# Kernel tuning notes

Measured on AMD Instinct MI355X. Metric: run time of the kernel, lower is better.

The kernel has to match this reference:

```python
import jax, jax.numpy as jnp
import numpy as np

B, T, I, H = 1024, 64, 64, 1024
FUTURE = 16


def lstm_cell(x_t, h, c, Wih, Whh, b_ih, b_hh):
    # torch LSTMCell gate order: i, f, g, o; weights are (4H, in)
    gates = x_t @ Wih.T + h @ Whh.T + b_ih + b_hh  # (B, 4H)
    i, f, g, o = jnp.split(gates, 4, axis=-1)
    i = jax.nn.sigmoid(i)
    f = jax.nn.sigmoid(f)
    g = jnp.tanh(g)
    o = jax.nn.sigmoid(o)
    c_new = f * c + i * g
    h_new = o * jnp.tanh(c_new)
    return h_new, c_new


def setup_inputs() -> dict:
    key = jax.random.key(0)
    ks = jax.random.split(key, 12)
    s1 = 1.0 / np.sqrt(H)
    inp = {
        "x": jax.random.normal(ks[0], (B, T, I), dtype=jnp.float32),
        "W_ih1": jax.random.uniform(ks[1], (4 * H, I), jnp.float32, -s1, s1),
        "W_hh1": jax.random.uniform(ks[2], (4 * H, H), jnp.float32, -s1, s1),
        "b_ih1": jax.random.uniform(ks[3], (4 * H,), jnp.float32, -s1, s1),
        "b_hh1": jax.random.uniform(ks[4], (4 * H,), jnp.float32, -s1, s1),
        "W_ih2": jax.random.uniform(ks[5], (4 * H, H), jnp.float32, -s1, s1),
        "W_hh2": jax.random.uniform(ks[6], (4 * H, H), jnp.float32, -s1, s1),
        "b_ih2": jax.random.uniform(ks[7], (4 * H,), jnp.float32, -s1, s1),
        "b_hh2": jax.random.uniform(ks[8], (4 * H,), jnp.float32, -s1, s1),
        "W_lin": jax.random.uniform(ks[9], (I, H), jnp.float32, -s1, s1),
        "b_lin": jax.random.uniform(ks[10], (I,), jnp.float32, -s1, s1),
        "future": FUTURE,
    }
    return inp


def reference(x, W_ih1, W_hh1, b_ih1, b_hh1, W_ih2, W_hh2, b_ih2, b_hh2,
              W_lin, b_lin, future):
    b_size = x.shape[0]
    zeros = jnp.zeros((b_size, H), dtype=x.dtype)

    def two_layer_step(h1, c1, h2, c2, x_t):
        h1, c1 = lstm_cell(x_t, h1, c1, W_ih1, W_hh1, b_ih1, b_hh1)
        h2, c2 = lstm_cell(h1, h2, c2, W_ih2, W_hh2, b_ih2, b_hh2)
        out = h2 @ W_lin.T + b_lin  # (B, I)
        return h1, c1, h2, c2, out

    def step(carry, x_t):
        h1, c1, h2, c2 = carry
        h1, c1, h2, c2, out = two_layer_step(h1, c1, h2, c2, x_t)
        return (h1, c1, h2, c2), out

    xs = jnp.transpose(x, (1, 0, 2))  # (T, B, I)
    carry, outs = jax.lax.scan(step, (zeros, zeros, zeros, zeros), xs)

    if future > 0:
        def fstep(carry, _):
            h1, c1, h2, c2, out = carry
            h1, c1, h2, c2, out = two_layer_step(h1, c1, h2, c2, out)
            return (h1, c1, h2, c2, out), out

        h1, c1, h2, c2 = carry
        _, fouts = jax.lax.scan(fstep, (h1, c1, h2, c2, outs[-1]),
                                None, length=future)
        outs = jnp.concatenate([outs, fouts], axis=0)

    return jnp.transpose(outs, (1, 0, 2))  # (B, T+future, I)
```

## Files before the change

### kernel.cpp

```cpp
#include <hip/hip_runtime.h>


#define B_   1024
#define T_   64
#define I_   64
#define H_   1024
#define FUT_ 16
#define NST_ (T_ + FUT_)
#define SROW 2176

typedef _Float16 half8_t  __attribute__((ext_vector_type(8)));
typedef float    float4_t __attribute__((ext_vector_type(4)));

__device__ __forceinline__ float sigmoid_f(float x) {
    x = fminf(fmaxf(x, -30.f), 30.f);
    return __fdividef(1.f, 1.f + __expf(-x));
}
__device__ __forceinline__ float tanh_f(float x) {
    x = fminf(fmaxf(x, -15.f), 15.f);
    float e = __expf(2.f * x);
    return 1.f - 2.f * __fdividef(1.f, e + 1.f);
}

__global__ void convert_all(const float* __restrict__ x,
    const float* __restrict__ Wih1, const float* __restrict__ Whh1,
    const float* __restrict__ bih1, const float* __restrict__ bhh1,
    const float* __restrict__ Wih2, const float* __restrict__ Whh2,
    const float* __restrict__ bih2, const float* __restrict__ bhh2,
    const float* __restrict__ Wlin,
    _Float16* __restrict__ W1p, _Float16* __restrict__ W2p,
    _Float16* __restrict__ Wlp,
    _Float16* __restrict__ S0x, _Float16* __restrict__ S1x,
    float* __restrict__ b1, float* __restrict__ b2)
{
    size_t idx = (size_t)blockIdx.x * 256 + threadIdx.x;
    const size_t nc1 = 589824;
    const size_t nc2 = 1048576;
    const size_t nc3 = 8192;
    const size_t nx  = 65536;
    if (idx < nc1) {
        int c = (int)idx;
        int lane = c & 63, g = (c >> 6) & 3, rem = c >> 8;
        int j = rem % 36, hgrp = rem / 36;
        int row = (g << 10) + hgrp * 16 + (lane & 15);
        int kb = j * 32 + (lane >> 4) * 8;
        _Float16* o = &W1p[(size_t)c * 8];
        if (kb < 1024) {
            #pragma unroll
            for (int i = 0; i < 8; ++i) o[i] = (_Float16)Whh1[(size_t)row * 1024 + kb + i];
        } else if (kb < 1088) {
            #pragma unroll
            for (int i = 0; i < 8; ++i) o[i] = (_Float16)Wih1[row * 64 + (kb - 1024) + i];
        } else {
            #pragma unroll
            for (int i = 0; i < 8; ++i) o[i] = (_Float16)0.f;
        }
    } else if ((idx -= nc1) < nc2) {
        int c = (int)idx;
        int lane = c & 63, g = (c >> 6) & 3, rem = c >> 8;
        int j = rem & 63, hgrp = rem >> 6;
        int row = (g << 10) + hgrp * 16 + (lane & 15);
        int kb = j * 32 + (lane >> 4) * 8;
        _Float16* o = &W2p[(size_t)c * 8];
        if (kb < 1024) {
            #pragma unroll
            for (int i = 0; i < 8; ++i) o[i] = (_Float16)Wih2[(size_t)row * 1024 + kb + i];
        } else {
            #pragma unroll
            for (int i = 0; i < 8; ++i) o[i] = (_Float16)Whh2[(size_t)row * 1024 + kb - 1024 + i];
        }
    } else if ((idx -= nc2) < nc3) {
        int c = (int)idx;
        int lane = c & 63, j = (c >> 6) & 31, hgrp = c >> 11;
        int row = hgrp * 16 + (lane & 15);
        int kb = j * 32 + (lane >> 4) * 8;
        _Float16* o = &Wlp[(size_t)c * 8];
        #pragma unroll
        for (int i = 0; i < 8; ++i) o[i] = (_Float16)Wlin[(size_t)row * 1024 + kb + i];
    } else if ((idx -= nc3) < nx) {
        int b = (int)(idx >> 6), i = (int)(idx & 63);
        S0x[(size_t)b * SROW + i] = (_Float16)x[(size_t)b * (T_ * I_) + i];
    } else if ((idx -= nx) < nx) {
        int b = (int)(idx >> 6), i = (int)(idx & 63);
        S1x[(size_t)b * SROW + i] = (_Float16)x[(size_t)b * (T_ * I_) + 64 + i];
    } else if ((idx -= nx) < 4096) {
        b1[idx] = bih1[idx] + bhh1[idx];
    } else if ((idx -= 4096) < 4096) {
        b2[idx] = bih2[idx] + bhh2[idx];
    }
}

__device__ __forceinline__ void gemm_body(_Float16 (*sA)[136],
    const _Float16* __restrict__ Alo, const _Float16* __restrict__ Ahi,
    const _Float16* __restrict__ Wp, const int iters, const int Ksh,
    const float* __restrict__ bias, float* __restrict__ cvec,
    _Float16* __restrict__ hdst, const int unit)
{
    const int tid = threadIdx.x;
    const int lane = tid & 63, w = tid >> 6;
    const int hw = w & 1, kh = w >> 1;
    const int lr = lane & 15, lq = lane >> 4;
    const int ht = unit & 31, mt = unit >> 5;
    const int h0 = ht * 32, m0 = mt * 64;
    const int hgrp = ht * 2 + hw;

    const char* wptr = (const char*)Wp
        + ((size_t)hgrp * (2 * Ksh) + (size_t)kh * Ksh) * 4096
        + (size_t)lane * 16;

    const int srow0 = tid >> 4, grp = tid & 15;
    const _Float16* abase = (grp < 8 ? Alo : Ahi) + (size_t)(grp & 7) * 8;
    const _Float16* arow = abase + (size_t)(m0 + srow0) * SROW;

    float4_t acc[4][4];
    #pragma unroll
    for (int g = 0; g < 4; ++g)
        #pragma unroll
        for (int rt = 0; rt < 4; ++rt)
            #pragma unroll
            for (int e = 0; e < 4; ++e) acc[g][rt][e] = 0.f;

    for (int i = 0; i < iters; ++i) {
        #pragma unroll
        for (int s = 0; s < 4; ++s)
            *(half8_t*)&sA[srow0 + s * 16][grp * 8] =
                *(const half8_t*)(arow + (size_t)s * 16 * SROW + i * 64);
        __syncthreads();
        #pragma unroll
        for (int ks = 0; ks < 2; ++ks) {
            half8_t af[4], bf[4];
            #pragma unroll
            for (int g = 0; g < 4; ++g)
                bf[g] = *(const half8_t*)(wptr + (ks * 4 + g) * 1024);
            #pragma unroll
            for (int rt = 0; rt < 4; ++rt)
                af[rt] = *(const half8_t*)&sA[rt * 16 + lr][kh * 64 + ks * 32 + lq * 8];
            #pragma unroll
            for (int g = 0; g < 4; ++g)
                #pragma unroll
                for (int rt = 0; rt < 4; ++rt)
                    acc[g][rt] = __builtin_amdgcn_mfma_f32_16x16x32_f16(
                        af[rt], bf[g], acc[g][rt], 0, 0, 0);
        }
        wptr += 8192;
        __syncthreads();
    }

    float* scr = (float*)&sA[0][0];
    #pragma unroll
    for (int gp = 0; gp < 2; ++gp) {
        if (kh == 1) {
            #pragma unroll
            for (int g2 = 0; g2 < 2; ++g2)
                #pragma unroll
                for (int rt = 0; rt < 4; ++rt) {
                    int slot = ((hw * 2 + g2) * 4 + rt) * 64 + lane;
                    *(float4_t*)&scr[slot * 4] = acc[gp * 2 + g2][rt];
                }
        }
        __syncthreads();
        if (kh == 0) {
            #pragma unroll
            for (int g2 = 0; g2 < 2; ++g2)
                #pragma unroll
                for (int rt = 0; rt < 4; ++rt) {
                    int slot = ((hw * 2 + g2) * 4 + rt) * 64 + lane;
                    acc[gp * 2 + g2][rt] += *(const float4_t*)&scr[slot * 4];
                }
        }
        __syncthreads();
    }
    if (kh != 0) return;

    const int j = h0 + hw * 16 + lr;
    const float bi = bias[j], bff = bias[1024 + j];
    const float bg = bias[2048 + j], bo = bias[3072 + j];
    #pragma unroll
    for (int rt = 0; rt < 4; ++rt) {
        #pragma unroll
        for (int e = 0; e < 4; ++e) {
            const int brow = m0 + rt * 16 + lq * 4 + e;
            float gi = sigmoid_f(acc[0][rt][e] + bi);
            float gf = sigmoid_f(acc[1][rt][e] + bff);
            float gg = tanh_f(acc[2][rt][e] + bg);
            float go = sigmoid_f(acc[3][rt][e] + bo);
            const size_t ci = (size_t)brow * 1024 + j;
            float cn = gf * cvec[ci] + gi * gg;
            cvec[ci] = cn;
            hdst[(size_t)brow * SROW + j] = (_Float16)(go * tanh_f(cn));
        }
    }
}

__device__ __forceinline__ void proj_body(_Float16 (*sA)[136],
    const _Float16* __restrict__ A, const _Float16* __restrict__ Wp,
    const float* __restrict__ blin, float* __restrict__ outp,
    _Float16* __restrict__ xdst, const int unit)
{
    const int iters = 8, Ksh = 16;
    const int tid = threadIdx.x;
    const int lane = tid & 63, w = tid >> 6;
    const int hw = w & 1, kh = w >> 1;
    const int lr = lane & 15, lq = lane >> 4;
    const int ht = unit & 1, mt = unit >> 1;
    const int h0 = ht * 32, m0 = mt * 64;
    const int hgrp = ht * 2 + hw;

    const char* wptr = (const char*)Wp
        + ((size_t)hgrp * (2 * Ksh) + (size_t)kh * Ksh) * 1024
        + (size_t)lane * 16;

    const int srow0 = tid >> 4, grp = tid & 15;
    const _Float16* abase = A + (grp >> 3) * 512 + (size_t)(grp & 7) * 8;
    const _Float16* arow = abase + (size_t)(m0 + srow0) * SROW;

    float4_t acc[4];
    #pragma unroll
    for (int rt = 0; rt < 4; ++rt)
        #pragma unroll
        for (int e = 0; e < 4; ++e) acc[rt][e] = 0.f;

    for (int i = 0; i < iters; ++i) {
        #pragma unroll
        for (int s = 0; s < 4; ++s)
            *(half8_t*)&sA[srow0 + s * 16][grp * 8] =
                *(const half8_t*)(arow + (size_t)s * 16 * SROW + i * 64);
        __syncthreads();
        #pragma unroll
        for (int ks = 0; ks < 2; ++ks) {
            half8_t af[4], bf;
            bf = *(const half8_t*)(wptr + ks * 1024);
            #pragma unroll
            for (int rt = 0; rt < 4; ++rt)
                af[rt] = *(const half8_t*)&sA[rt * 16 + lr][kh * 64 + ks * 32 + lq * 8];
            #pragma unroll
            for (int rt = 0; rt < 4; ++rt)
                acc[rt] = __builtin_amdgcn_mfma_f32_16x16x32_f16(
                    af[rt], bf, acc[rt], 0, 0, 0);
        }
        wptr += 2048;
        __syncthreads();
    }

    float* scr = (float*)&sA[0][0];
    if (kh == 1) {
        #pragma unroll
        for (int rt = 0; rt < 4; ++rt) {
            int slot = (hw * 4 + rt) * 64 + lane;
            *(float4_t*)&scr[slot * 4] = acc[rt];
        }
    }
    __syncthreads();
    if (kh != 0) return;
    #pragma unroll
    for (int rt = 0; rt < 4; ++rt) {
        int slot = (hw * 4 + rt) * 64 + lane;
        acc[rt] += *(const float4_t*)&scr[slot * 4];
    }

    const int j = h0 + hw * 16 + lr;
    const float bj = blin[j];
    #pragma unroll
    for (int rt = 0; rt < 4; ++rt) {
        #pragma unroll
        for (int e = 0; e < 4; ++e) {
            const int brow = m0 + rt * 16 + lq * 4 + e;
            float s = acc[rt][e] + bj;
            outp[(size_t)brow * (NST_ * I_) + j] = s;
            if (xdst) xdst[(size_t)brow * SROW + j] = (_Float16)s;
        }
    }
}

struct StepArgs {
    int nL2, nL1, nProj, nCopy;
    const _Float16 *l2Alo, *l2Ahi; _Float16* l2H; float* c2;
    const _Float16 *l1Alo, *l1Ahi; _Float16* l1H; float* c1;
    const _Float16* pA; float* pOut; _Float16* pXdst;
    const float* xsrc; _Float16* xdst;
    const _Float16 *W1p, *W2p, *Wlp;
    const float *b1, *b2, *blin;
};

__global__ __launch_bounds__(256, 4) void fused_step(StepArgs a) {
    __shared__ __align__(16) _Float16 sA[64][136];
    int bid = blockIdx.x;
    if (bid < a.nL2) {
        gemm_body(sA, a.l2Alo, a.l2Ahi, a.W2p, 16, 32, a.b2, a.c2, a.l2H, bid);
    } else if ((bid -= a.nL2) < a.nL1) {
        gemm_body(sA, a.l1Alo, a.l1Ahi, a.W1p, 9, 18, a.b1, a.c1, a.l1H, bid);
    } else if ((bid -= a.nL1) < a.nProj) {
        proj_body(sA, a.pA, a.Wlp, a.blin, a.pOut, a.pXdst, bid);
    } else {
        bid -= a.nProj;
        int base = bid * 256 + threadIdx.x;
        for (int k = base; k < B_ * I_; k += a.nCopy * 256) {
            int b = k >> 6, i = k & 63;
            a.xdst[(size_t)b * SROW + i] = (_Float16)a.xsrc[(size_t)b * (T_ * I_) + i];
        }
    }
}

extern "C" void kernel_launch(void* const* d_in, const int* in_sizes, int n_in,
                              void* d_out, int out_size, void* d_ws, size_t ws_size,
                              hipStream_t stream) {
    (void)in_sizes; (void)n_in; (void)out_size; (void)ws_size;
    const float* x    = (const float*)d_in[0];
    const float* Wih1 = (const float*)d_in[1];
    const float* Whh1 = (const float*)d_in[2];
    const float* bih1 = (const float*)d_in[3];
    const float* bhh1 = (const float*)d_in[4];
    const float* Wih2 = (const float*)d_in[5];
    const float* Whh2 = (const float*)d_in[6];
    const float* bih2 = (const float*)d_in[7];
    const float* bhh2 = (const float*)d_in[8];
    const float* Wlin = (const float*)d_in[9];
    const float* blin = (const float*)d_in[10];
    float* out = (float*)d_out;

    char* p = (char*)d_ws;
    auto alloc = [&](size_t bytes) {
        char* r = p; p += (bytes + 255) & ~(size_t)255; return r;
    };
    _Float16* W1p = (_Float16*)alloc((size_t)4096 * 1152 * 2);
    _Float16* W2p = (_Float16*)alloc((size_t)4096 * 2048 * 2);
    _Float16* Wlp = (_Float16*)alloc((size_t)64 * 1024 * 2);
    _Float16* S[3];
    for (int i = 0; i < 3; ++i) S[i] = (_Float16*)alloc((size_t)B_ * SROW * 2);
    float* c1 = (float*)alloc((size_t)B_ * H_ * 4);
    float* c2 = (float*)alloc((size_t)B_ * H_ * 4);
    float* b1 = (float*)alloc(4096 * 4);
    float* b2 = (float*)alloc(4096 * 4);

    for (int i = 0; i < 3; ++i)
        hipMemsetAsync(S[i], 0, (size_t)B_ * SROW * 2, stream);
    hipMemsetAsync(c1, 0, (size_t)B_ * H_ * 4, stream);
    hipMemsetAsync(c2, 0, (size_t)B_ * H_ * 4, stream);

    {
        const size_t total = 589824 + 1048576 + 8192 + 65536 + 65536 + 8192;
        convert_all<<<(int)((total + 255) / 256), 256, 0, stream>>>(
            x, Wih1, Whh1, bih1, bhh1, Wih2, Whh2, bih2, bhh2, Wlin,
            W1p, W2p, Wlp, S[0] + 1024, S[1] + 1024, b1, b2);
    }

    StepArgs a{};
    a.W1p = W1p; a.W2p = W2p; a.Wlp = Wlp;
    a.b1 = b1; a.b2 = b2; a.blin = blin;
    a.c1 = c1; a.c2 = c2;

    {
        StepArgs q = a;
        q.nL2 = 0; q.nL1 = 512; q.nProj = 0; q.nCopy = 0;
        q.l1Alo = S[0]; q.l1Ahi = S[0] + 576; q.l1H = S[1];
        fused_step<<<512, 256, 0, stream>>>(q);
    }

    for (int t = 0; t <= 62; ++t) {
        _Float16* Sp = S[t % 3];
        _Float16* Sq = S[(t + 1) % 3];
        _Float16* Sn = S[(t + 2) % 3];
        StepArgs q = a;
        q.nL2 = 512; q.nL1 = 512;
        q.nProj = (t >= 1) ? 32 : 0;
        q.nCopy = (t <= 61) ? 16 : 0;
        q.l2Alo = Sq; q.l2Ahi = Sp + 1152; q.l2H = Sq + 1152;
        q.l1Alo = Sq; q.l1Ahi = Sq + 576; q.l1H = Sn;
        q.pA = Sp + 1152; q.pOut = out + (size_t)(t - 1) * I_; q.pXdst = nullptr;
        q.xsrc = x + (size_t)(t + 2) * I_; q.xdst = Sn + 1024;
        int grid = q.nL2 + q.nL1 + q.nProj + q.nCopy;
        fused_step<<<grid, 256, 0, stream>>>(q);
    }

    {
        StepArgs q = a;
        q.nL2 = 512; q.nL1 = 0; q.nProj = 32; q.nCopy = 0;
        q.l2Alo = S[1]; q.l2Ahi = S[0] + 1152; q.l2H = S[1] + 1152;
        q.pA = S[0] + 1152; q.pOut = out + (size_t)62 * I_; q.pXdst = nullptr;
        fused_step<<<544, 256, 0, stream>>>(q);
    }
    {
        StepArgs q = a;
        q.nL2 = 0; q.nL1 = 0; q.nProj = 32; q.nCopy = 0;
        q.pA = S[1] + 1152; q.pOut = out + (size_t)63 * I_; q.pXdst = S[1] + 1024;
        fused_step<<<32, 256, 0, stream>>>(q);
    }

    for (int t = T_; t < NST_; ++t) {
        _Float16* Sp = S[t % 3];
        _Float16* Sq = S[(t + 1) % 3];
        {
            StepArgs q = a;
            q.nL2 = 0; q.nL1 = 512; q.nProj = 0; q.nCopy = 0;
            q.l1Alo = Sp; q.l1Ahi = Sp + 576; q.l1H = Sq;
            fused_step<<<512, 256, 0, stream>>>(q);
        }
        {
            StepArgs q = a;
            q.nL2 = 512; q.nL1 = 0; q.nProj = 0; q.nCopy = 0;
            q.l2Alo = Sq; q.l2Ahi = Sp + 1152; q.l2H = Sq + 1152;
            fused_step<<<512, 256, 0, stream>>>(q);
        }
        {
            StepArgs q = a;
            q.nL2 = 0; q.nL1 = 0; q.nProj = 32; q.nCopy = 0;
            q.pA = Sq + 1152; q.pOut = out + (size_t)t * I_;
            q.pXdst = (t + 1 < NST_) ? (Sq + 1024) : nullptr;
            fused_step<<<32, 256, 0, stream>>>(q);
        }
    }
}
```

Before: 3.771 ms.

## Stage A tiles via direct global-to-LDS loads, prefetch weights, swizzle LDS

The activation tiles are now staged into shared memory with global_load_lds (direct-to-LDS DMA) into an unpadded, XOR-swizzled layout rather than going through registers. The next iteration's weight fragments are loaded into registers one iteration ahead so global latency overlaps the MFMAs. The mapping from block index to hidden tile is permuted, and launch bounds drop to 3 waves per SIMD to leave room for the extra registers. The aim is to hide load latency and avoid LDS bank conflicts, at the cost of more register pressure and lower occupancy.

```diff
diff --git a/kernel.cpp b/kernel.cpp
--- a/kernel.cpp
+++ b/kernel.cpp
@@ -11,6 +11,13 @@
 
 typedef _Float16 half8_t  __attribute__((ext_vector_type(8)));
 typedef float    float4_t __attribute__((ext_vector_type(4)));
+
+typedef __attribute__((address_space(1))) const unsigned int g_u32;
+typedef __attribute__((address_space(3))) unsigned int l_u32;
+
+__device__ __forceinline__ void load_lds16(const _Float16* g, _Float16* l) {
+    __builtin_amdgcn_global_load_lds((g_u32*)g, (l_u32*)l, 16, 0, 0);
+}
 
 __device__ __forceinline__ float sigmoid_f(float x) {
     x = fminf(fmaxf(x, -30.f), 30.f);
@@ -90,7 +97,7 @@
     }
 }
 
-__device__ __forceinline__ void gemm_body(_Float16 (*sA)[136],
+__device__ __forceinline__ void gemm_body(_Float16* sA,
     const _Float16* __restrict__ Alo, const _Float16* __restrict__ Ahi,
     const _Float16* __restrict__ Wp, const int iters, const int Ksh,
     const float* __restrict__ bias, float* __restrict__ cvec,
@@ -100,7 +107,8 @@
     const int lane = tid & 63, w = tid >> 6;
     const int hw = w & 1, kh = w >> 1;
     const int lr = lane & 15, lq = lane >> 4;
-    const int ht = unit & 31, mt = unit >> 5;
+    const int ht = ((unit & 7) << 2) | ((unit >> 3) & 3);
+    const int mt = unit >> 5;
     const int h0 = ht * 32, m0 = mt * 64;
     const int hgrp = ht * 2 + hw;
 
@@ -108,9 +116,14 @@
         + ((size_t)hgrp * (2 * Ksh) + (size_t)kh * Ksh) * 4096
         + (size_t)lane * 16;
 
-    const int srow0 = tid >> 4, grp = tid & 15;
-    const _Float16* abase = (grp < 8 ? Alo : Ahi) + (size_t)(grp & 7) * 8;
-    const _Float16* arow = abase + (size_t)(m0 + srow0) * SROW;
+    const int srow0 = tid >> 4, pg = tid & 15;
+    const int gg = pg ^ (srow0 & 15);
+    const _Float16* asrc = (gg < 8 ? Alo : Ahi) + (gg & 7) * 8
+                         + (size_t)(m0 + srow0) * SROW;
+    _Float16* ldst = sA + tid * 8;
+
+    const int ag0 = ((kh * 8 + lq) ^ lr) * 8;
+    const int ag1 = ((kh * 8 + 4 + lq) ^ lr) * 8;
 
     float4_t acc[4][4];
     #pragma unroll
@@ -120,33 +133,46 @@
             #pragma unroll
             for (int e = 0; e < 4; ++e) acc[g][rt][e] = 0.f;
 
+    half8_t bfc[8], bfn[8];
+    #pragma unroll
+    for (int q = 0; q < 8; ++q)
+        bfc[q] = *(const half8_t*)(wptr + q * 1024);
+
     for (int i = 0; i < iters; ++i) {
         #pragma unroll
         for (int s = 0; s < 4; ++s)
-            *(half8_t*)&sA[srow0 + s * 16][grp * 8] =
-                *(const half8_t*)(arow + (size_t)s * 16 * SROW + i * 64);
-        __syncthreads();
+            load_lds16(asrc + (size_t)(srow0 + s * 16 - srow0) * 0
+                       + (size_t)s * 16 * SROW + (size_t)i * 64,
+                       ldst + s * 2048);
+        __syncthreads();
+
+        if (i + 1 < iters) {
+            const char* wn = wptr + 8192;
+            #pragma unroll
+            for (int q = 0; q < 8; ++q)
+                bfn[q] = *(const half8_t*)(wn + q * 1024);
+        }
         #pragma unroll
         for (int ks = 0; ks < 2; ++ks) {
-            half8_t af[4], bf[4];
-            #pragma unroll
-            for (int g = 0; g < 4; ++g)
-                bf[g] = *(const half8_t*)(wptr + (ks * 4 + g) * 1024);
+            const int ag = ks ? ag1 : ag0;
+            half8_t af[4];
             #pragma unroll
             for (int rt = 0; rt < 4; ++rt)
-                af[rt] = *(const half8_t*)&sA[rt * 16 + lr][kh * 64 + ks * 32 + lq * 8];
+                af[rt] = *(const half8_t*)&sA[(rt * 16 + lr) * 128 + ag];
             #pragma unroll
             for (int g = 0; g < 4; ++g)
                 #pragma unroll
                 for (int rt = 0; rt < 4; ++rt)
                     acc[g][rt] = __builtin_amdgcn_mfma_f32_16x16x32_f16(
-                        af[rt], bf[g], acc[g][rt], 0, 0, 0);
-        }
+                        af[rt], bfc[ks * 4 + g], acc[g][rt], 0, 0, 0);
+        }
+        __syncthreads();
         wptr += 8192;
-        __syncthreads();
-    }
-
-    float* scr = (float*)&sA[0][0];
+        #pragma unroll
+        for (int q = 0; q < 8; ++q) bfc[q] = bfn[q];
+    }
+
+    float* scr = (float*)sA;
     #pragma unroll
     for (int gp = 0; gp < 2; ++gp) {
         if (kh == 1) {
@@ -182,22 +208,22 @@
             const int brow = m0 + rt * 16 + lq * 4 + e;
             float gi = sigmoid_f(acc[0][rt][e] + bi);
             float gf = sigmoid_f(acc[1][rt][e] + bff);
-            float gg = tanh_f(acc[2][rt][e] + bg);
+            float gv = tanh_f(acc[2][rt][e] + bg);
             float go = sigmoid_f(acc[3][rt][e] + bo);
             const size_t ci = (size_t)brow * 1024 + j;
-            float cn = gf * cvec[ci] + gi * gg;
+            float cn = gf * cvec[ci] + gi * gv;
             cvec[ci] = cn;
             hdst[(size_t)brow * SROW + j] = (_Float16)(go * tanh_f(cn));
         }
     }
 }
 
-__device__ __forceinline__ void proj_body(_Float16 (*sA)[136],
+__device__ __forceinline__ void proj_body(_Float16* sA,
     const _Float16* __restrict__ A, const _Float16* __restrict__ Wp,
     const float* __restrict__ blin, float* __restrict__ outp,
     _Float16* __restrict__ xdst, const int unit)
 {
-    const int iters = 8, Ksh = 16;
+    const int iters = 8;
     const int tid = threadIdx.x;
     const int lane = tid & 63, w = tid >> 6;
     const int hw = w & 1, kh = w >> 1;
@@ -207,12 +233,15 @@
     const int hgrp = ht * 2 + hw;
 
     const char* wptr = (const char*)Wp
-        + ((size_t)hgrp * (2 * Ksh) + (size_t)kh * Ksh) * 1024
-        + (size_t)lane * 16;
-
-    const int srow0 = tid >> 4, grp = tid & 15;
-    const _Float16* abase = A + (grp >> 3) * 512 + (size_t)(grp & 7) * 8;
-    const _Float16* arow = abase + (size_t)(m0 + srow0) * SROW;
+        + ((size_t)hgrp * 32 + (size_t)kh * 16) * 1024 + (size_t)lane * 16;
+
+    const int srow0 = tid >> 4, pg = tid & 15;
+    const int gg = pg ^ (srow0 & 15);
+    const _Float16* asrc = A + (size_t)(gg >> 3) * 512 + (gg & 7) * 8
+                         + (size_t)(m0 + srow0) * SROW;
+    _Float16* ldst = sA + tid * 8;
+    const int ag0 = ((kh * 8 + lq) ^ lr) * 8;
+    const int ag1 = ((kh * 8 + 4 + lq) ^ lr) * 8;
 
     float4_t acc[4];
     #pragma unroll
@@ -220,29 +249,36 @@
         #pragma unroll
         for (int e = 0; e < 4; ++e) acc[rt][e] = 0.f;
 
+    half8_t b0 = *(const half8_t*)(wptr);
+    half8_t b1v = *(const half8_t*)(wptr + 1024);
     for (int i = 0; i < iters; ++i) {
         #pragma unroll
         for (int s = 0; s < 4; ++s)
-            *(half8_t*)&sA[srow0 + s * 16][grp * 8] =
-                *(const half8_t*)(arow + (size_t)s * 16 * SROW + i * 64);
-        __syncthreads();
-        #pragma unroll
-        for (int ks = 0; ks < 2; ++ks) {
-            half8_t af[4], bf;
-            bf = *(const half8_t*)(wptr + ks * 1024);
-            #pragma unroll
-            for (int rt = 0; rt < 4; ++rt)
-                af[rt] = *(const half8_t*)&sA[rt * 16 + lr][kh * 64 + ks * 32 + lq * 8];
-            #pragma unroll
-            for (int rt = 0; rt < 4; ++rt)
-                acc[rt] = __builtin_amdgcn_mfma_f32_16x16x32_f16(
-                    af[rt], bf, acc[rt], 0, 0, 0);
-        }
+            load_lds16(asrc + (size_t)s * 16 * SROW + (size_t)i * 64,
+                       ldst + s * 2048);
+        __syncthreads();
+        half8_t n0, n1;
+        if (i + 1 < iters) {
+            n0 = *(const half8_t*)(wptr + 2048);
+            n1 = *(const half8_t*)(wptr + 3072);
+        }
+        half8_t af;
+        #pragma unroll
+        for (int rt = 0; rt < 4; ++rt) {
+            af = *(const half8_t*)&sA[(rt * 16 + lr) * 128 + ag0];
+            acc[rt] = __builtin_amdgcn_mfma_f32_16x16x32_f16(af, b0, acc[rt], 0, 0, 0);
+        }
+        #pragma unroll
+        for (int rt = 0; rt < 4; ++rt) {
+            af = *(const half8_t*)&sA[(rt * 16 + lr) * 128 + ag1];
+            acc[rt] = __builtin_amdgcn_mfma_f32_16x16x32_f16(af, b1v, acc[rt], 0, 0, 0);
+        }
+        __syncthreads();
         wptr += 2048;
-        __syncthreads();
-    }
-
-    float* scr = (float*)&sA[0][0];
+        b0 = n0; b1v = n1;
+    }
+
+    float* scr = (float*)sA;
     if (kh == 1) {
         #pragma unroll
         for (int rt = 0; rt < 4; ++rt) {
@@ -282,8 +318,8 @@
     const float *b1, *b2, *blin;
 };
 
-__global__ __launch_bounds__(256, 4) void fused_step(StepArgs a) {
-    __shared__ __align__(16) _Float16 sA[64][136];
+__global__ __launch_bounds__(256, 3) void fused_step(StepArgs a) {
+    __shared__ __align__(16) _Float16 sA[8192];
     int bid = blockIdx.x;
     if (bid < a.nL2) {
         gemm_body(sA, a.l2Alo, a.l2Ahi, a.W2p, 16, 32, a.b2, a.c2, a.l2H, bid);
```

After: 3.686 ms. 1.02x faster.
